# Performance work log

Hardware: AMD Instinct MI355X
Metric: run time of the kernel (lower is better)

Reference implementation:

```python
import jax, jax.numpy as jnp
import numpy as np

N = 40000
E = 640000
IN_FEATS = 128
OUT_FEATS = 64
K = 8
FACTOR_DIM = OUT_FEATS // K  # 8
ITERATIONS = 3
TAU = 1.0
LEAKY_SLOPE = 0.01  # torch nn.LeakyReLU default


def setup_inputs() -> dict:
    key = jax.random.key(0)
    k1, k2, k3 = jax.random.split(key, 3)
    x = jax.random.normal(k1, (N, IN_FEATS), dtype=jnp.float32)
    # xavier_normal_ with gain=1.414: std = gain * sqrt(2 / (fan_in + fan_out))
    std = 1.414 * np.sqrt(2.0 / (IN_FEATS + OUT_FEATS))
    weight = jax.random.normal(k2, (IN_FEATS, OUT_FEATS), dtype=jnp.float32) * std
    bias = jnp.zeros((OUT_FEATS,), dtype=jnp.float32)
    edge_index = jax.random.randint(k3, (2, E), 0, N, dtype=jnp.int32)
    return {"x": x, "weight": weight, "bias": bias, "edge_index": edge_index}


def _l2norm(h):
    # h / ||h||_2 along last dim (no eps, matching torch code)
    return h / jnp.sqrt((h * h).sum(-1, keepdims=True))


def reference(x, weight, bias, edge_index):
    num_nodes = x.shape[0]
    src = edge_index[0]  # scatter target / softmax segment node
    dst = edge_index[1]  # gathered neighbor node

    h = jax.nn.leaky_relu(x @ weight + bias, LEAKY_SLOPE)          # [N, out]
    # split into K factors of FACTOR_DIM: [N, K, d]
    h = h.reshape(num_nodes, K, FACTOR_DIM)
    h_normed = _l2norm(h)                                           # [N, K, d]

    h_src = h_normed
    h_dst = h_normed
    for _ in range(ITERATIONS):
        feat_nbr = h_src[dst]                                       # [E, K, d]
        s = (h_dst[src] * feat_nbr).sum(-1) / TAU                   # [E, K]
        # segment softmax over edges grouped by src node
        smax = jax.ops.segment_max(s, src, num_segments=num_nodes)  # [N, K]
        ex = jnp.exp(s - smax[src])                                 # [E, K]
        denom = jax.ops.segment_sum(ex, src, num_segments=num_nodes)
        alpha = ex / denom[src]                                     # [E, K]
        msg = feat_nbr * alpha[..., None]                           # [E, K, d]
        node_attr = jax.ops.segment_sum(msg, src, num_segments=num_nodes)
        node_attr = node_attr + h_normed                            # [N, K, d]
        h_dst = _l2norm(node_attr)
    return h_dst.reshape(num_nodes, -1)                             # [N, out]
```

## Files before the change

kernel.cpp:

```cpp
#include <hip/hip_runtime.h>
#include <math.h>

#define NN   40000
#define EE   640000
#define INF_ 128
#define OUTF 64
#define SLOTS 64

#define NBUCK 313
#define NCOLS 625
#define NBINS (NBUCK * NCOLS)
#define SCANA_BLOCKS ((NBINS + 255) / 256)

typedef float f2 __attribute__((ext_vector_type(2)));

__device__ __forceinline__ f2 pkfma(f2 a, f2 b, f2 c) {
    return __builtin_elementwise_fma(a, b, c);
}
__device__ __forceinline__ f2 shf2(f2 a, int m) {
    f2 b; b.x = __shfl_xor(a.x, m); b.y = __shfl_xor(a.y, m); return b;
}
__device__ __forceinline__ f2 bfpair(unsigned u) {
    f2 c;
    c.x = __uint_as_float(u << 16);
    c.y = __uint_as_float(u & 0xffff0000u);
    return c;
}
__device__ __forceinline__ unsigned short f2bf(float f) {
    unsigned u = __float_as_uint(f);
    return (unsigned short)((u + 0x7fffu + ((u >> 16) & 1u)) >> 16);
}


__global__ __launch_bounds__(256) void count_gemm_k(
        const float* __restrict__ x, const float* __restrict__ w,
        const float* __restrict__ bias, float* __restrict__ hn,
        unsigned short* __restrict__ hn16,
        const int4* __restrict__ src4, int* __restrict__ binsT,
        uchar4* __restrict__ lrank4) {
    __shared__ float wl[INF_ * OUTF];
    __shared__ float xl[4][8 * 132];

    if (blockIdx.x < NCOLS) {
        int b = blockIdx.x;
        int* lbin = (int*)wl;
        for (int i = threadIdx.x; i < NBUCK; i += 256) lbin[i] = 0;
        __syncthreads();
        int t = b * 256 + threadIdx.x;
        int4 s = src4[t];
        uchar4 lr;
        lr.x = (unsigned char)atomicAdd(&lbin[s.x >> 7], 1);
        lr.y = (unsigned char)atomicAdd(&lbin[s.y >> 7], 1);
        lr.z = (unsigned char)atomicAdd(&lbin[s.z >> 7], 1);
        lr.w = (unsigned char)atomicAdd(&lbin[s.w >> 7], 1);
        lrank4[t] = lr;
        __syncthreads();
        for (int u = threadIdx.x; u < NBUCK; u += 256) binsT[u * NCOLS + b] = lbin[u];
        return;
    }

    for (int i = threadIdx.x; i < INF_ * OUTF; i += 256) wl[i] = w[i];

    int wv = threadIdx.x >> 6;
    int l  = threadIdx.x & 63;
    int q  = l >> 4;
    int rr = l & 15;
    float4 bv = ((const float4*)bias)[rr];
    int srow = l >> 5;
    int scol = (l & 31) * 4;

    int nb = ((blockIdx.x - NCOLS) * 4 + wv) * 16;

#pragma unroll
    for (int h = 0; h < 2; ++h) {
        int n0 = nb + h * 8;
        {
            const float4* xs = (const float4*)(x + (size_t)n0 * INF_);
#pragma unroll
            for (int j = 0; j < 4; ++j) {
                float4 v = xs[j * 64 + l];
                *(float4*)&xl[wv][(j * 2 + srow) * 132 + scol] = v;
            }
        }
        if (h == 0) __syncthreads();
        float4 a0 = bv, a1 = bv;
        const float* x0 = &xl[wv][q * 132];
        const float* x1 = &xl[wv][(q + 4) * 132];
#pragma unroll 4
        for (int i = 0; i < INF_; ++i) {
            float4 w4 = ((const float4*)wl)[i * 16 + rr];
            float xv0 = x0[i], xv1 = x1[i];
            a0.x = fmaf(xv0, w4.x, a0.x); a0.y = fmaf(xv0, w4.y, a0.y);
            a0.z = fmaf(xv0, w4.z, a0.z); a0.w = fmaf(xv0, w4.w, a0.w);
            a1.x = fmaf(xv1, w4.x, a1.x); a1.y = fmaf(xv1, w4.y, a1.y);
            a1.z = fmaf(xv1, w4.z, a1.z); a1.w = fmaf(xv1, w4.w, a1.w);
        }
        a0.x = a0.x > 0.f ? a0.x : 0.01f * a0.x;
        a0.y = a0.y > 0.f ? a0.y : 0.01f * a0.y;
        a0.z = a0.z > 0.f ? a0.z : 0.01f * a0.z;
        a0.w = a0.w > 0.f ? a0.w : 0.01f * a0.w;
        a1.x = a1.x > 0.f ? a1.x : 0.01f * a1.x;
        a1.y = a1.y > 0.f ? a1.y : 0.01f * a1.y;
        a1.z = a1.z > 0.f ? a1.z : 0.01f * a1.z;
        a1.w = a1.w > 0.f ? a1.w : 0.01f * a1.w;
        float s0 = a0.x*a0.x + a0.y*a0.y + a0.z*a0.z + a0.w*a0.w;
        float s1 = a1.x*a1.x + a1.y*a1.y + a1.z*a1.z + a1.w*a1.w;
        s0 += __shfl_xor(s0, 1);
        s1 += __shfl_xor(s1, 1);
        float v0 = rsqrtf(s0), v1 = rsqrtf(s1);
        float4 o0 = make_float4(a0.x*v0, a0.y*v0, a0.z*v0, a0.w*v0);
        float4 o1 = make_float4(a1.x*v1, a1.y*v1, a1.z*v1, a1.w*v1);
        ((float4*)hn)[(size_t)(n0 + q) * 16 + rr] = o0;
        ((float4*)hn)[(size_t)(n0 + 4 + q) * 16 + rr] = o1;
        ushort4 u0, u1;
        u0.x = f2bf(o0.x); u0.y = f2bf(o0.y); u0.z = f2bf(o0.z); u0.w = f2bf(o0.w);
        u1.x = f2bf(o1.x); u1.y = f2bf(o1.y); u1.z = f2bf(o1.z); u1.w = f2bf(o1.w);
        ((ushort4*)hn16)[(size_t)(n0 + q) * 16 + rr] = u0;
        ((ushort4*)hn16)[(size_t)(n0 + 4 + q) * 16 + rr] = u1;
    }
}


__global__ void scanA_k(const int* __restrict__ binsT, int* __restrict__ excl,
                        int* __restrict__ bsum) {
    __shared__ int tmp[256];
    int i = blockIdx.x * 256 + threadIdx.x;
    int v = (i < NBINS) ? binsT[i] : 0;
    tmp[threadIdx.x] = v;
    __syncthreads();
    for (int off = 1; off < 256; off <<= 1) {
        int t = (threadIdx.x >= off) ? tmp[threadIdx.x - off] : 0;
        __syncthreads();
        tmp[threadIdx.x] += t;
        __syncthreads();
    }
    if (i < NBINS) excl[i] = tmp[threadIdx.x] - v;
    if (threadIdx.x == 255) bsum[blockIdx.x] = tmp[255];
}

__global__ __launch_bounds__(1024) void scanB_k(int* __restrict__ bsum) {
    __shared__ int tmp[1024];
    int v = (threadIdx.x < SCANA_BLOCKS) ? bsum[threadIdx.x] : 0;
    tmp[threadIdx.x] = v;
    __syncthreads();
    for (int off = 1; off < 1024; off <<= 1) {
        int t = (threadIdx.x >= off) ? tmp[threadIdx.x - off] : 0;
        __syncthreads();
        tmp[threadIdx.x] += t;
        __syncthreads();
    }
    if (threadIdx.x < SCANA_BLOCKS) bsum[threadIdx.x] = tmp[threadIdx.x] - v;
}


__global__ __launch_bounds__(256) void part_k(const int4* __restrict__ src4,
                                              const int4* __restrict__ dst4,
                                              const uchar4* __restrict__ lrank4,
                                              const int* __restrict__ excl,
                                              const int* __restrict__ bsum,
                                              unsigned* __restrict__ part) {
    int b = blockIdx.x;
    int t = b * 256 + threadIdx.x;
    int4 s = src4[t];
    int4 d = dst4[t];
    uchar4 lr = lrank4[t];
    int i0 = (s.x >> 7) * NCOLS + b;
    int i1 = (s.y >> 7) * NCOLS + b;
    int i2 = (s.z >> 7) * NCOLS + b;
    int i3 = (s.w >> 7) * NCOLS + b;
    part[excl[i0] + bsum[i0 >> 8] + lr.x] = ((unsigned)d.x << 7) | (unsigned)(s.x & 127);
    part[excl[i1] + bsum[i1 >> 8] + lr.y] = ((unsigned)d.y << 7) | (unsigned)(s.y & 127);
    part[excl[i2] + bsum[i2 >> 8] + lr.z] = ((unsigned)d.z << 7) | (unsigned)(s.z & 127);
    part[excl[i3] + bsum[i3 >> 8] + lr.w] = ((unsigned)d.w << 7) | (unsigned)(s.w & 127);
}


__global__ __launch_bounds__(256) void attn_build_k(const uint4* __restrict__ hg,
                                                    const float* __restrict__ hnf,
                                                    float* __restrict__ out,
                                                    const unsigned* __restrict__ part,
                                                    const int* __restrict__ excl,
                                                    const int* __restrict__ bsum) {
    __shared__ unsigned short csr_l[32][SLOTS];
    __shared__ int cnt[32];

    int u = blockIdx.x >> 2;
    int c = blockIdx.x & 3;
    if (threadIdx.x < 32) cnt[threadIdx.x] = 0;
    __syncthreads();

    int iu = u * NCOLS;
    int beg = excl[iu] + bsum[iu >> 8];
    int end = EE;
    if (u + 1 < NBUCK) {
        int iv = (u + 1) * NCOLS;
        end = excl[iv] + bsum[iv >> 8];
    }
    for (int e = beg + threadIdx.x; e < end; e += 256) {
        unsigned p = part[e];
        int lo = (int)(p & 127u);
        if ((lo >> 5) == c) {
            int lr = atomicAdd(&cnt[lo & 31], 1);
            if (lr < SLOTS) csr_l[lo & 31][lr] = (unsigned short)(p >> 7);
        }
    }
    __syncthreads();

    int wv = threadIdx.x >> 6;
    int l  = threadIdx.x & 63;
    int pp_ = l >> 5, q = (l >> 3) & 3, r = l & 7;
    int nbase = u * 128 + c * 32;

#pragma unroll
    for (int pass = 0; pass < 4; ++pass) {
        int ln = pass * 8 + wv * 2 + pp_;
        int n  = nbase + ln;
        if (n >= NN) continue;

        const unsigned short* row = csr_l[ln];
        int deg = min(cnt[ln], SLOTS);

        bool k0 = q      < deg;
        bool k1 = q + 4  < deg;
        bool k2 = q + 8  < deg;
        bool k3 = q + 12 < deg;
        bool k4 = q + 16 < deg;
        bool k5 = q + 20 < deg;
        bool k6 = q + 24 < deg;
        bool k7 = q + 28 < deg;
        unsigned i0 = min((unsigned)row[q     ], NN - 1u);
        unsigned i1 = min((unsigned)row[q +  4], NN - 1u);
        unsigned i2 = min((unsigned)row[q +  8], NN - 1u);
        unsigned i3 = min((unsigned)row[q + 12], NN - 1u);
        unsigned i4 = min((unsigned)row[q + 16], NN - 1u);
        unsigned i5 = min((unsigned)row[q + 20], NN - 1u);
        unsigned i6 = min((unsigned)row[q + 24], NN - 1u);
        unsigned i7 = min((unsigned)row[q + 28], NN - 1u);
        uint4 g0 = hg[(size_t)i0 * 8 + r];
        uint4 g1 = hg[(size_t)i1 * 8 + r];
        uint4 g2 = hg[(size_t)i2 * 8 + r];
        uint4 g3 = hg[(size_t)i3 * 8 + r];
        uint4 g4 = hg[(size_t)i4 * 8 + r];
        uint4 g5 = hg[(size_t)i5 * 8 + r];
        uint4 g6 = hg[(size_t)i6 * 8 + r];
        uint4 g7 = hg[(size_t)i7 * 8 + r];

        const float4* hs4 = (const float4*)(hnf + (size_t)n * OUTF + r * 8);
        float4 ha = hs4[0], hb = hs4[1];
        f2 hs01 = {ha.x, ha.y}, hs23 = {ha.z, ha.w};
        f2 hs45 = {hb.x, hb.y}, hs67 = {hb.z, hb.w};
        f2 hd01 = hs01, hd23 = hs23, hd45 = hs45, hd67 = hs67;

        for (int it = 0; it < 3; ++it) {
            float ssum = 0.f;
            f2 A0 = {0.f, 0.f}, A1 = A0, A2 = A0, A3 = A0;

            auto proc = [&](uint4 g, bool ok) {
                f2 c0 = bfpair(g.x), c1 = bfpair(g.y), c2 = bfpair(g.z), c3 = bfpair(g.w);
                f2 d = c0 * hd01;
                d = pkfma(c1, hd23, d);
                d = pkfma(c2, hd45, d);
                d = pkfma(c3, hd67, d);
                float dd = d.x + d.y;
                float ex = ok ? __expf(dd) : 0.f;
                ssum += ex;
                f2 exv = {ex, ex};
                A0 = pkfma(c0, exv, A0);
                A1 = pkfma(c1, exv, A1);
                A2 = pkfma(c2, exv, A2);
                A3 = pkfma(c3, exv, A3);
            };

            proc(g0, k0); proc(g1, k1); proc(g2, k2); proc(g3, k3);
            proc(g4, k4); proc(g5, k5); proc(g6, k6); proc(g7, k7);

            for (int e = 32 + q; e < deg; e += 4) {
                unsigned ii = min((unsigned)row[e], NN - 1u);
                proc(hg[(size_t)ii * 8 + r], true);
            }

#pragma unroll
            for (int m = 8; m < 32; m <<= 1) {
                ssum += __shfl_xor(ssum, m);
                A0 += shf2(A0, m);
                A1 += shf2(A1, m);
                A2 += shf2(A2, m);
                A3 += shf2(A3, m);
            }

            float rs = (ssum > 0.f) ? 1.f / ssum : 0.f;
            f2 rsv = {rs, rs};
            f2 t01 = pkfma(A0, rsv, hs01);
            f2 t23 = pkfma(A1, rsv, hs23);
            f2 t45 = pkfma(A2, rsv, hs45);
            f2 t67 = pkfma(A3, rsv, hs67);
            f2 d = t01 * t01;
            d = pkfma(t23, t23, d);
            d = pkfma(t45, t45, d);
            d = pkfma(t67, t67, d);
            float inv = rsqrtf(d.x + d.y);
            f2 iv = {inv, inv};
            hd01 = t01 * iv; hd23 = t23 * iv; hd45 = t45 * iv; hd67 = t67 * iv;
        }

        if (q == 0) {
            float4* o4 = (float4*)(out + (size_t)n * OUTF + r * 8);
            o4[0] = make_float4(hd01.x, hd01.y, hd23.x, hd23.y);
            o4[1] = make_float4(hd45.x, hd45.y, hd67.x, hd67.y);
        }
    }
}


extern "C" void kernel_launch(void* const* d_in, const int* in_sizes, int n_in,
                              void* d_out, int out_size, void* d_ws, size_t ws_size,
                              hipStream_t stream) {
    const float* x    = (const float*)d_in[0];
    const float* w    = (const float*)d_in[1];
    const float* bias = (const float*)d_in[2];
    const int*   ei   = (const int*)d_in[3];
    const int*   src  = ei;
    const int*   dst  = ei + EE;
    float* out = (float*)d_out;

    char* ws = (char*)d_ws;
    size_t off = 0;
    float*          hn    = (float*)(ws + off);          off += (size_t)NN * OUTF * 4;
    unsigned short* hn16  = (unsigned short*)(ws + off); off += (size_t)NN * OUTF * 2;
    int*            binsT = (int*)(ws + off);            off += (size_t)NBINS * 4 + 12;
    int*            excl  = (int*)(ws + off);            off += (size_t)NBINS * 4 + 12;
    int*            bsum  = (int*)(ws + off);            off += 4096;
    uchar4*         lrank = (uchar4*)(ws + off);         off += (size_t)EE;
    unsigned*       part  = (unsigned*)(ws + off);       off += (size_t)EE * 4;
    (void)ws_size; (void)in_sizes; (void)n_in; (void)out_size;

    count_gemm_k<<<NCOLS + 625, 256, 0, stream>>>(
        x, w, bias, hn, hn16, (const int4*)src, binsT, lrank);

    scanA_k<<<SCANA_BLOCKS, 256, 0, stream>>>(binsT, excl, bsum);
    scanB_k<<<1, 1024, 0, stream>>>(bsum);

    part_k<<<NCOLS, 256, 0, stream>>>((const int4*)src, (const int4*)dst,
                                      (const uchar4*)lrank, excl, bsum, part);

    attn_build_k<<<NBUCK * 4, 256, 0, stream>>>((const uint4*)hn16, hn, out,
                                                part, excl, bsum);
}
```

Before: 68.83 us.

## Fold spine scan into consumers, coarsen edge partition columns, hoist bf16 unpacking

Each counting and partition block now covers four times as many edges, which cuts the number of histogram columns and scan bins. The separate single-block spine-scan kernel is removed. Instead, part_k and attn_build_k each rescan the small block-sum array in shared memory, trading one kernel launch and one dependency for a little redundant work per block. The attention kernel also unpacks the bf16 neighbour features once, outside the three-iteration loop, and stops unrolling the pass loop. This saves repeated unpack ALU work at the cost of higher register pressure.

```diff
diff --git a/kernel.cpp b/kernel.cpp
--- a/kernel.cpp
+++ b/kernel.cpp
@@ -8,9 +8,10 @@
 #define SLOTS 64
 
 #define NBUCK 313
-#define NCOLS 625
+#define NCOLS 157
 #define NBINS (NBUCK * NCOLS)
 #define SCANA_BLOCKS ((NBINS + 255) / 256)
+#define NG4  (EE / 4)
 
 typedef float f2 __attribute__((ext_vector_type(2)));
 
@@ -46,14 +47,19 @@
         int* lbin = (int*)wl;
         for (int i = threadIdx.x; i < NBUCK; i += 256) lbin[i] = 0;
         __syncthreads();
-        int t = b * 256 + threadIdx.x;
-        int4 s = src4[t];
-        uchar4 lr;
-        lr.x = (unsigned char)atomicAdd(&lbin[s.x >> 7], 1);
-        lr.y = (unsigned char)atomicAdd(&lbin[s.y >> 7], 1);
-        lr.z = (unsigned char)atomicAdd(&lbin[s.z >> 7], 1);
-        lr.w = (unsigned char)atomicAdd(&lbin[s.w >> 7], 1);
-        lrank4[t] = lr;
+#pragma unroll
+        for (int rnd = 0; rnd < 4; ++rnd) {
+            int gi = b * 1024 + rnd * 256 + threadIdx.x;
+            if (gi < NG4) {
+                int4 s = src4[gi];
+                uchar4 lr;
+                lr.x = (unsigned char)atomicAdd(&lbin[s.x >> 7], 1);
+                lr.y = (unsigned char)atomicAdd(&lbin[s.y >> 7], 1);
+                lr.z = (unsigned char)atomicAdd(&lbin[s.z >> 7], 1);
+                lr.w = (unsigned char)atomicAdd(&lbin[s.w >> 7], 1);
+                lrank4[gi] = lr;
+            }
+        }
         __syncthreads();
         for (int u = threadIdx.x; u < NBUCK; u += 256) binsT[u * NCOLS + b] = lbin[u];
         return;
@@ -138,18 +144,18 @@
     if (threadIdx.x == 255) bsum[blockIdx.x] = tmp[255];
 }
 
-__global__ __launch_bounds__(1024) void scanB_k(int* __restrict__ bsum) {
-    __shared__ int tmp[1024];
+__device__ __forceinline__ void spine_scan(const int* __restrict__ bsum, int* spine) {
     int v = (threadIdx.x < SCANA_BLOCKS) ? bsum[threadIdx.x] : 0;
-    tmp[threadIdx.x] = v;
-    __syncthreads();
-    for (int off = 1; off < 1024; off <<= 1) {
-        int t = (threadIdx.x >= off) ? tmp[threadIdx.x - off] : 0;
-        __syncthreads();
-        tmp[threadIdx.x] += t;
-        __syncthreads();
-    }
-    if (threadIdx.x < SCANA_BLOCKS) bsum[threadIdx.x] = tmp[threadIdx.x] - v;
+    spine[threadIdx.x] = v;
+    __syncthreads();
+    for (int off = 1; off < 256; off <<= 1) {
+        int t = (threadIdx.x >= off) ? spine[threadIdx.x - off] : 0;
+        __syncthreads();
+        spine[threadIdx.x] += t;
+        __syncthreads();
+    }
+    spine[threadIdx.x] -= v;
+    __syncthreads();
 }
 
 
@@ -159,19 +165,27 @@
                                               const int* __restrict__ excl,
                                               const int* __restrict__ bsum,
                                               unsigned* __restrict__ part) {
+    __shared__ int spine[256];
+    spine_scan(bsum, spine);
+
     int b = blockIdx.x;
-    int t = b * 256 + threadIdx.x;
-    int4 s = src4[t];
-    int4 d = dst4[t];
-    uchar4 lr = lrank4[t];
-    int i0 = (s.x >> 7) * NCOLS + b;
-    int i1 = (s.y >> 7) * NCOLS + b;
-    int i2 = (s.z >> 7) * NCOLS + b;
-    int i3 = (s.w >> 7) * NCOLS + b;
-    part[excl[i0] + bsum[i0 >> 8] + lr.x] = ((unsigned)d.x << 7) | (unsigned)(s.x & 127);
-    part[excl[i1] + bsum[i1 >> 8] + lr.y] = ((unsigned)d.y << 7) | (unsigned)(s.y & 127);
-    part[excl[i2] + bsum[i2 >> 8] + lr.z] = ((unsigned)d.z << 7) | (unsigned)(s.z & 127);
-    part[excl[i3] + bsum[i3 >> 8] + lr.w] = ((unsigned)d.w << 7) | (unsigned)(s.w & 127);
+#pragma unroll
+    for (int rnd = 0; rnd < 4; ++rnd) {
+        int gi = b * 1024 + rnd * 256 + threadIdx.x;
+        if (gi < NG4) {
+            int4 s = src4[gi];
+            int4 d = dst4[gi];
+            uchar4 lr = lrank4[gi];
+            int i0 = (s.x >> 7) * NCOLS + b;
+            int i1 = (s.y >> 7) * NCOLS + b;
+            int i2 = (s.z >> 7) * NCOLS + b;
+            int i3 = (s.w >> 7) * NCOLS + b;
+            part[excl[i0] + spine[i0 >> 8] + lr.x] = ((unsigned)d.x << 7) | (unsigned)(s.x & 127);
+            part[excl[i1] + spine[i1 >> 8] + lr.y] = ((unsigned)d.y << 7) | (unsigned)(s.y & 127);
+            part[excl[i2] + spine[i2 >> 8] + lr.z] = ((unsigned)d.z << 7) | (unsigned)(s.z & 127);
+            part[excl[i3] + spine[i3 >> 8] + lr.w] = ((unsigned)d.w << 7) | (unsigned)(s.w & 127);
+        }
+    }
 }
 
 
@@ -183,6 +197,9 @@
                                                     const int* __restrict__ bsum) {
     __shared__ unsigned short csr_l[32][SLOTS];
     __shared__ int cnt[32];
+    __shared__ int spine[256];
+
+    spine_scan(bsum, spine);
 
     int u = blockIdx.x >> 2;
     int c = blockIdx.x & 3;
@@ -190,11 +207,11 @@
     __syncthreads();
 
     int iu = u * NCOLS;
-    int beg = excl[iu] + bsum[iu >> 8];
+    int beg = excl[iu] + spine[iu >> 8];
     int end = EE;
     if (u + 1 < NBUCK) {
         int iv = (u + 1) * NCOLS;
-        end = excl[iv] + bsum[iv >> 8];
+        end = excl[iv] + spine[iv >> 8];
     }
     for (int e = beg + threadIdx.x; e < end; e += 256) {
         unsigned p = part[e];
@@ -211,7 +228,7 @@
     int pp_ = l >> 5, q = (l >> 3) & 3, r = l & 7;
     int nbase = u * 128 + c * 32;
 
-#pragma unroll
+#pragma unroll 1
     for (int pass = 0; pass < 4; ++pass) {
         int ln = pass * 8 + wv * 2 + pp_;
         int n  = nbase + ln;
@@ -245,6 +262,15 @@
         uint4 g6 = hg[(size_t)i6 * 8 + r];
         uint4 g7 = hg[(size_t)i7 * 8 + r];
 
+        f2 e0c0 = bfpair(g0.x), e0c1 = bfpair(g0.y), e0c2 = bfpair(g0.z), e0c3 = bfpair(g0.w);
+        f2 e1c0 = bfpair(g1.x), e1c1 = bfpair(g1.y), e1c2 = bfpair(g1.z), e1c3 = bfpair(g1.w);
+        f2 e2c0 = bfpair(g2.x), e2c1 = bfpair(g2.y), e2c2 = bfpair(g2.z), e2c3 = bfpair(g2.w);
+        f2 e3c0 = bfpair(g3.x), e3c1 = bfpair(g3.y), e3c2 = bfpair(g3.z), e3c3 = bfpair(g3.w);
+        f2 e4c0 = bfpair(g4.x), e4c1 = bfpair(g4.y), e4c2 = bfpair(g4.z), e4c3 = bfpair(g4.w);
+        f2 e5c0 = bfpair(g5.x), e5c1 = bfpair(g5.y), e5c2 = bfpair(g5.z), e5c3 = bfpair(g5.w);
+        f2 e6c0 = bfpair(g6.x), e6c1 = bfpair(g6.y), e6c2 = bfpair(g6.z), e6c3 = bfpair(g6.w);
+        f2 e7c0 = bfpair(g7.x), e7c1 = bfpair(g7.y), e7c2 = bfpair(g7.z), e7c3 = bfpair(g7.w);
+
         const float4* hs4 = (const float4*)(hnf + (size_t)n * OUTF + r * 8);
         float4 ha = hs4[0], hb = hs4[1];
         f2 hs01 = {ha.x, ha.y}, hs23 = {ha.z, ha.w};
@@ -255,8 +281,7 @@
             float ssum = 0.f;
             f2 A0 = {0.f, 0.f}, A1 = A0, A2 = A0, A3 = A0;
 
-            auto proc = [&](uint4 g, bool ok) {
-                f2 c0 = bfpair(g.x), c1 = bfpair(g.y), c2 = bfpair(g.z), c3 = bfpair(g.w);
+            auto proc = [&](f2 c0, f2 c1, f2 c2, f2 c3, bool ok) {
                 f2 d = c0 * hd01;
                 d = pkfma(c1, hd23, d);
                 d = pkfma(c2, hd45, d);
@@ -271,12 +296,19 @@
                 A3 = pkfma(c3, exv, A3);
             };
 
-            proc(g0, k0); proc(g1, k1); proc(g2, k2); proc(g3, k3);
-            proc(g4, k4); proc(g5, k5); proc(g6, k6); proc(g7, k7);
+            proc(e0c0, e0c1, e0c2, e0c3, k0);
+            proc(e1c0, e1c1, e1c2, e1c3, k1);
+            proc(e2c0, e2c1, e2c2, e2c3, k2);
+            proc(e3c0, e3c1, e3c2, e3c3, k3);
+            proc(e4c0, e4c1, e4c2, e4c3, k4);
+            proc(e5c0, e5c1, e5c2, e5c3, k5);
+            proc(e6c0, e6c1, e6c2, e6c3, k6);
+            proc(e7c0, e7c1, e7c2, e7c3, k7);
 
             for (int e = 32 + q; e < deg; e += 4) {
                 unsigned ii = min((unsigned)row[e], NN - 1u);
-                proc(hg[(size_t)ii * 8 + r], true);
+                uint4 g = hg[(size_t)ii * 8 + r];
+                proc(bfpair(g.x), bfpair(g.y), bfpair(g.z), bfpair(g.w), true);
             }
 
 #pragma unroll
@@ -329,7 +361,7 @@
     unsigned short* hn16  = (unsigned short*)(ws + off); off += (size_t)NN * OUTF * 2;
     int*            binsT = (int*)(ws + off);            off += (size_t)NBINS * 4 + 12;
     int*            excl  = (int*)(ws + off);            off += (size_t)NBINS * 4 + 12;
-    int*            bsum  = (int*)(ws + off);            off += 4096;
+    int*            bsum  = (int*)(ws + off);            off += 1024;
     uchar4*         lrank = (uchar4*)(ws + off);         off += (size_t)EE;
     unsigned*       part  = (unsigned*)(ws + off);       off += (size_t)EE * 4;
     (void)ws_size; (void)in_sizes; (void)n_in; (void)out_size;
@@ -338,7 +370,6 @@
         x, w, bias, hn, hn16, (const int4*)src, binsT, lrank);
 
     scanA_k<<<SCANA_BLOCKS, 256, 0, stream>>>(binsT, excl, bsum);
-    scanB_k<<<1, 1024, 0, stream>>>(bsum);
 
     part_k<<<NCOLS, 256, 0, stream>>>((const int4*)src, (const int4*)dst,
                                       (const uchar4*)lrank, excl, bsum, part);
```

New measurement: 68.49 us. No clear change (-0.5%).
